# Kernel optimization log

Measured on AMD Instinct MI355X. Metric: run time of the kernel, lower is better.

Reference implementation:

```python
import jax, jax.numpy as jnp
import numpy as np

N_TOKENS = 16384
DIM = 2048
N_EXPERTS = 64
TOPK = 8
ROUTE_SCALE = 1.0


def setup_inputs() -> dict:
    key = jax.random.key(0)
    k1, k2 = jax.random.split(key)
    x = jax.random.normal(k1, (N_TOKENS, DIM), dtype=jnp.float32)
    W = jax.random.normal(k2, (N_EXPERTS, DIM), dtype=jnp.float32) * 0.02
    return {"x": x, "W": W}


def reference(x, W):
    # linear scores: [tokens, n_experts]
    logits = jnp.einsum('td,ed->te', x, W)
    # softmax in float32 (score_func == 'softmax'); bias is None since dim != 64
    scores = jax.nn.softmax(logits.astype(jnp.float32), axis=-1)
    # top-k expert selection, then gather original scores at selected indices
    _, indices = jax.lax.top_k(scores, TOPK)
    weights = jnp.take_along_axis(scores, indices, axis=-1)
    # softmax path: no renormalization, just route scaling
    weights = (weights * ROUTE_SCALE).astype(x.dtype)
    return weights, indices
```

## Files before the change

kernel.cpp:

```cpp
#include <hip/hip_runtime.h>


typedef __attribute__((ext_vector_type(8))) short short8;
typedef __attribute__((ext_vector_type(16))) float f32x16;
typedef __attribute__((ext_vector_type(4))) float f32x4;
typedef __attribute__((ext_vector_type(4))) unsigned int u32x4;

#define NT    16384
#define DIMK  2048
#define NE    64
#define TOPKK 8
#define WPK_BYTES 786432
#define PL_BYTES  (4 * NT * NE * 4)
#define WS_NEED   (WPK_BYTES + PL_BYTES)

union U4S8 { unsigned int u[4]; short8 s; u32x4 v; };

__device__ __forceinline__ short8 as_s8(u32x4 v) { U4S8 t; t.v = v; return t.s; }

__device__ __forceinline__ void split3(const float4 a, const float4 b,
                                       short8& H, short8& M, short8& L) {
    const float f[8] = {a.x, a.y, a.z, a.w, b.x, b.y, b.z, b.w};
    U4S8 uh, um, ul;
#pragma unroll
    for (int p = 0; p < 4; ++p) {
        const float f0 = f[2 * p], f1 = f[2 * p + 1];
        const unsigned int t0 = __float_as_uint(f0) & 0xFFFF0000u;
        const unsigned int t1 = __float_as_uint(f1) & 0xFFFF0000u;
        uh.u[p] = (t0 >> 16) | t1;
        const float r0 = f0 - __uint_as_float(t0);
        const float r1 = f1 - __uint_as_float(t1);
        const unsigned int v0 = __float_as_uint(r0) & 0xFFFF0000u;
        const unsigned int v1 = __float_as_uint(r1) & 0xFFFF0000u;
        um.u[p] = (v0 >> 16) | v1;
        const float s0 = r0 - __uint_as_float(v0);
        const float s1 = r1 - __uint_as_float(v1);
        ul.u[p] = (__float_as_uint(s0) >> 16) | (__float_as_uint(s1) & 0xFFFF0000u);
    }
    H = uh.s; M = um.s; L = ul.s;
}

__device__ __forceinline__ f32x16 mfma6w(short8 ah, short8 am, short8 al,
                                         short8 bh, short8 bm, short8 bl,
                                         f32x16 c) {
    c = __builtin_amdgcn_mfma_f32_32x32x16_bf16(ah, bh, c, 0, 0, 0);
    c = __builtin_amdgcn_mfma_f32_32x32x16_bf16(ah, bm, c, 0, 0, 0);
    c = __builtin_amdgcn_mfma_f32_32x32x16_bf16(am, bh, c, 0, 0, 0);
    c = __builtin_amdgcn_mfma_f32_32x32x16_bf16(ah, bl, c, 0, 0, 0);
    c = __builtin_amdgcn_mfma_f32_32x32x16_bf16(am, bm, c, 0, 0, 0);
    c = __builtin_amdgcn_mfma_f32_32x32x16_bf16(al, bh, c, 0, 0, 0);
    return c;
}

__global__ __launch_bounds__(64) void pack_w_kernel(
    const float* __restrict__ W, short* __restrict__ wpk)
{
    const int b  = blockIdx.x;
    const int c  = b >> 3, fg = b & 7;
    const int s  = fg >> 1, n32 = fg & 1;
    const int l  = threadIdx.x;
    const float* g = W + (size_t)(32 * n32 + (l & 31)) * DIMK
                       + 64 * c + 16 * s + 8 * (l >> 5);
    const float4 lo = *(const float4*)g;
    const float4 hi = *(const float4*)(g + 4);
    short8 H, M, L;
    split3(lo, hi, H, M, L);
    const size_t base = ((size_t)(c * 8 + fg) * 3) * 512 + l * 8;
    *(short8*)(wpk + base)        = H;
    *(short8*)(wpk + base + 512)  = M;
    *(short8*)(wpk + base + 1024) = L;
}

#define WLOAD3(d0, d1, d2, p)                                                 \
    asm volatile("global_load_dwordx4 %0, %3, off\n\t"                        \
                 "global_load_dwordx4 %1, %3, off offset:1024\n\t"            \
                 "global_load_dwordx4 %2, %3, off offset:2048"                \
                 : "=&v"(d0), "=&v"(d1), "=&v"(d2) : "v"(p))
#define WAITN(n) do {                                                         \
    asm volatile("s_waitcnt vmcnt(" #n ")" ::: "memory");                     \
    __builtin_amdgcn_sched_barrier(0);                                        \
} while (0)

__device__ __forceinline__ void async16(void* lds, const void* gp) {
    __builtin_amdgcn_global_load_lds(
        (const __attribute__((address_space(1))) unsigned int*)gp,
        (__attribute__((address_space(3))) unsigned int*)lds, 16, 0, 0);
}

__global__ __launch_bounds__(512, 1) void gate_ksplit_kernel(
    const float* __restrict__ x, const short* __restrict__ wpk,
    float* __restrict__ pl)
{
    __shared__ __align__(16) char smem[8 * 3 * 4096];

    const int tid = threadIdx.x;
    const int w   = tid >> 6;
    const int l   = tid & 63;
    const int r31 = l & 31;
    const int l5  = l >> 5;
    const int tg  = blockIdx.x >> 2;
    const int kq  = blockIdx.x & 3;
    const int bt0 = tg * 256;
    const int tokbase = bt0 + 32 * w;

    char* wbase = smem + w * 12288;
    const int swr = (r31 & 7) ^ (((r31 >> 3) & 3) << 1);
    const int srow = l >> 3;
    const int sg0  = (l & 7) ^ srow;
    const float* xrow0 = x + (size_t)(tokbase + srow) * DIMK + kq * 512;

#define STAGE_CHUNK(k) do {                                                   \
    _Pragma("unroll")                                                         \
    for (int i = 0; i < 4; ++i) {                                             \
        const float* gsrc = xrow0 + (size_t)(8 * i) * DIMK + (k) * 32         \
                          + ((sg0 ^ (2 * i)) << 2);                           \
        async16(wbase + ((k) % 3) * 4096 + i * 1024, gsrc);                   \
    }                                                                         \
} while (0)

    const short* wq0 = wpk + (size_t)kq * 98304 + l * 8;
    const short* wq1 = wq0 + 1536;

    f32x16 acc0, acc1;
#pragma unroll
    for (int i = 0; i < 16; ++i) { acc0[i] = 0.f; acc1[i] = 0.f; }

    u32x4 w0v[4][3], w1v[4][3];

    STAGE_CHUNK(0);
    STAGE_CHUNK(1);
    STAGE_CHUNK(2);
    WLOAD3(w0v[0][0], w0v[0][1], w0v[0][2], wq0); wq0 += 3072;
    WLOAD3(w1v[0][0], w1v[0][1], w1v[0][2], wq1); wq1 += 3072;
    WLOAD3(w0v[1][0], w0v[1][1], w0v[1][2], wq0); wq0 += 3072;
    WLOAD3(w1v[1][0], w1v[1][1], w1v[1][2], wq1); wq1 += 3072;
    WLOAD3(w0v[2][0], w0v[2][1], w0v[2][2], wq0); wq0 += 3072;
    WLOAD3(w1v[2][0], w1v[2][1], w1v[2][2], wq1); wq1 += 3072;

#define SLICE(t) do {                                                         \
    if ((t) <= 28) {                                                          \
        WLOAD3(w0v[((t)+3)&3][0], w0v[((t)+3)&3][1], w0v[((t)+3)&3][2], wq0); \
        wq0 += 3072;                                                          \
        WLOAD3(w1v[((t)+3)&3][0], w1v[((t)+3)&3][1], w1v[((t)+3)&3][2], wq1); \
        wq1 += 3072;                                                          \
    }                                                                         \
    if ((t) <= 1)            WAITN(18);                                       \
    else if ((t) == 29)      WAITN(12);                                       \
    else if ((t) == 30)      WAITN(6);                                        \
    else if ((t) == 31)      WAITN(0);                                        \
    else if (((t) & 1) || (t) == 2 || (t) == 28) WAITN(22);                   \
    else                     WAITN(26);                                       \
    {                                                                         \
        const char* xb = wbase + (((t) >> 1) % 3) * 4096;                     \
        const float4 a0 = *(const float4*)(xb + r31 * 128 +                   \
            (((((t) & 1) * 4 + 2 * l5 + 0) ^ swr) << 4));                     \
        const float4 a1 = *(const float4*)(xb + r31 * 128 +                   \
            (((((t) & 1) * 4 + 2 * l5 + 1) ^ swr) << 4));                     \
        short8 H, M, L;                                                       \
        split3(a0, a1, H, M, L);                                              \
        acc0 = mfma6w(H, M, L, as_s8(w0v[(t)&3][0]), as_s8(w0v[(t)&3][1]),    \
                      as_s8(w0v[(t)&3][2]), acc0);                            \
        acc1 = mfma6w(H, M, L, as_s8(w1v[(t)&3][0]), as_s8(w1v[(t)&3][1]),    \
                      as_s8(w1v[(t)&3][2]), acc1);                            \
    }                                                                         \
    if (((t) & 1) && (t) <= 25) STAGE_CHUNK(((t) + 5) >> 1);                  \
} while (0)

#define PBAR() __builtin_amdgcn_s_barrier()

    SLICE(0);  SLICE(1);  PBAR();
    SLICE(2);  SLICE(3);  PBAR();
    SLICE(4);  SLICE(5);  PBAR();
    SLICE(6);  SLICE(7);  PBAR();
    SLICE(8);  SLICE(9);  PBAR();
    SLICE(10); SLICE(11); PBAR();
    SLICE(12); SLICE(13); PBAR();
    SLICE(14); SLICE(15); PBAR();
    SLICE(16); SLICE(17); PBAR();
    SLICE(18); SLICE(19); PBAR();
    SLICE(20); SLICE(21); PBAR();
    SLICE(22); SLICE(23); PBAR();
    SLICE(24); SLICE(25); PBAR();
    SLICE(26); SLICE(27); PBAR();
    SLICE(28); SLICE(29); PBAR();
    SLICE(30); SLICE(31);

    float* base0 = pl + ((size_t)kq * NT + tokbase) * NE;
#pragma unroll
    for (int r = 0; r < 16; ++r) {
        const int rowc = (r & 3) + 8 * (r >> 2) + 4 * l5;
        base0[rowc * NE + r31]      = acc0[r];
        base0[rowc * NE + 32 + r31] = acc1[r];
    }
#undef SLICE
#undef STAGE_CHUNK
#undef PBAR
}

__global__ __launch_bounds__(128) void gate_combine_kernel(
    const float* __restrict__ pl, float* __restrict__ out)
{
    __shared__ float lgs[128][NE + 1];

    const int tid = threadIdx.x;
    const int t0  = blockIdx.x * 128;

#pragma unroll
    for (int i = 0; i < 16; ++i) {
        const int idx = i * 128 + tid;
        const int tok = idx >> 4, c4 = idx & 15;
        const size_t off = ((size_t)t0 + tok) * NE + c4 * 4;
        const f32x4 v0 = *(const f32x4*)(pl + off);
        const f32x4 v1 = *(const f32x4*)(pl + (size_t)NT * NE + off);
        const f32x4 v2 = *(const f32x4*)(pl + (size_t)2 * NT * NE + off);
        const f32x4 v3 = *(const f32x4*)(pl + (size_t)3 * NT * NE + off);
        const f32x4 s = (v0 + v1) + (v2 + v3);
#pragma unroll
        for (int j = 0; j < 4; ++j) lgs[tok][c4 * 4 + j] = s[j];
    }
    __syncthreads();

    const float* rowp = &lgs[tid][0];
    float mx = -3.402823466e38f;
    for (int e = 0; e < NE; ++e) mx = fmaxf(mx, rowp[e]);
    float sden = 0.f;
    for (int e = 0; e < NE; ++e) sden += expf(rowp[e] - mx);

    float tv[TOPKK];
    int   ti[TOPKK];
#pragma unroll
    for (int i = 0; i < TOPKK; ++i) { tv[i] = -3.402823466e38f; ti[i] = 0; }
    for (int e = 0; e < NE; ++e) {
        const float v = rowp[e];
        if (v > tv[TOPKK - 1]) {
            tv[TOPKK - 1] = v; ti[TOPKK - 1] = e;
#pragma unroll
            for (int q = TOPKK - 1; q > 0; --q) {
                if (tv[q] > tv[q - 1]) {
                    const float fv = tv[q]; tv[q] = tv[q - 1]; tv[q - 1] = fv;
                    const int   iv = ti[q]; ti[q] = ti[q - 1]; ti[q - 1] = iv;
                }
            }
        }
    }

    float* ow = out + (size_t)(t0 + tid) * TOPKK;
    float* oi = out + (size_t)NT * TOPKK + (size_t)(t0 + tid) * TOPKK;
#pragma unroll
    for (int i = 0; i < TOPKK; ++i) {
        ow[i] = expf(tv[i] - mx) / sden;
        oi[i] = (float)ti[i];
    }
}

__global__ __launch_bounds__(512, 1) void gate_main_r8(
    const float* __restrict__ x, const short* __restrict__ wpk,
    float* __restrict__ out)
{
    __shared__ __align__(16) char smem[8 * 3 * 4096];
    const int tid = threadIdx.x;
    const int w   = tid >> 6;
    const int l   = tid & 63;
    const int r31 = l & 31;
    const int l5  = l >> 5;
    const int tw  = w & 1;
    const int kq  = w >> 1;
    const int bt0 = blockIdx.x * 64;
    char* wbase = smem + w * 12288;
    const int swr = (r31 & 7) ^ (((r31 >> 3) & 3) << 1);
    const int srow = l >> 3;
    const int sg0  = (l & 7) ^ srow;
    const float* xrow0 = x + (size_t)(bt0 + 32 * tw + srow) * DIMK + kq * 512;

#define STAGE_CHUNK(k) do {                                                   \
    _Pragma("unroll")                                                         \
    for (int i = 0; i < 4; ++i) {                                             \
        const float* gsrc = xrow0 + (size_t)(8 * i) * DIMK + (k) * 32         \
                          + ((sg0 ^ (2 * i)) << 2);                           \
        async16(wbase + ((k) % 3) * 4096 + i * 1024, gsrc);                   \
    }                                                                         \
} while (0)

    const short* wq0 = wpk + (size_t)kq * 98304 + l * 8;
    const short* wq1 = wq0 + 1536;
    f32x16 acc0, acc1;
#pragma unroll
    for (int i = 0; i < 16; ++i) { acc0[i] = 0.f; acc1[i] = 0.f; }
    u32x4 w0v[4][3], w1v[4][3];
    STAGE_CHUNK(0); STAGE_CHUNK(1); STAGE_CHUNK(2);
    WLOAD3(w0v[0][0], w0v[0][1], w0v[0][2], wq0); wq0 += 3072;
    WLOAD3(w1v[0][0], w1v[0][1], w1v[0][2], wq1); wq1 += 3072;
    WLOAD3(w0v[1][0], w0v[1][1], w0v[1][2], wq0); wq0 += 3072;
    WLOAD3(w1v[1][0], w1v[1][1], w1v[1][2], wq1); wq1 += 3072;
    WLOAD3(w0v[2][0], w0v[2][1], w0v[2][2], wq0); wq0 += 3072;
    WLOAD3(w1v[2][0], w1v[2][1], w1v[2][2], wq1); wq1 += 3072;

#define SLICE(t) do {                                                         \
    if ((t) <= 28) {                                                          \
        WLOAD3(w0v[((t)+3)&3][0], w0v[((t)+3)&3][1], w0v[((t)+3)&3][2], wq0); \
        wq0 += 3072;                                                          \
        WLOAD3(w1v[((t)+3)&3][0], w1v[((t)+3)&3][1], w1v[((t)+3)&3][2], wq1); \
        wq1 += 3072;                                                          \
    }                                                                         \
    if ((t) <= 1)            WAITN(18);                                       \
    else if ((t) == 29)      WAITN(12);                                       \
    else if ((t) == 30)      WAITN(6);                                        \
    else if ((t) == 31)      WAITN(0);                                        \
    else if (((t) & 1) || (t) == 2 || (t) == 28) WAITN(22);                   \
    else                     WAITN(26);                                       \
    {                                                                         \
        const char* xb = wbase + (((t) >> 1) % 3) * 4096;                     \
        const float4 a0 = *(const float4*)(xb + r31 * 128 +                   \
            (((((t) & 1) * 4 + 2 * l5 + 0) ^ swr) << 4));                     \
        const float4 a1 = *(const float4*)(xb + r31 * 128 +                   \
            (((((t) & 1) * 4 + 2 * l5 + 1) ^ swr) << 4));                     \
        short8 H, M, L;                                                       \
        split3(a0, a1, H, M, L);                                              \
        acc0 = mfma6w(H, M, L, as_s8(w0v[(t)&3][0]), as_s8(w0v[(t)&3][1]),    \
                      as_s8(w0v[(t)&3][2]), acc0);                            \
        acc1 = mfma6w(H, M, L, as_s8(w1v[(t)&3][0]), as_s8(w1v[(t)&3][1]),    \
                      as_s8(w1v[(t)&3][2]), acc1);                            \
    }                                                                         \
    if (((t) & 1) && (t) <= 25) STAGE_CHUNK(((t) + 5) >> 1);                  \
} while (0)

    SLICE(0);  SLICE(1);  SLICE(2);  SLICE(3);
    SLICE(4);  SLICE(5);  SLICE(6);  SLICE(7);
    SLICE(8);  SLICE(9);  SLICE(10); SLICE(11);
    SLICE(12); SLICE(13); SLICE(14); SLICE(15);
    SLICE(16); SLICE(17); SLICE(18); SLICE(19);
    SLICE(20); SLICE(21); SLICE(22); SLICE(23);
    SLICE(24); SLICE(25); SLICE(26); SLICE(27);
    SLICE(28); SLICE(29); SLICE(30); SLICE(31);

    __syncthreads();
    float* lg = (float*)smem;
#pragma unroll
    for (int r = 0; r < 16; ++r) {
        const int rowc = (r & 3) + 8 * (r >> 2) + 4 * l5;
        const int trow = 32 * tw + rowc;
        lg[(kq * 64 + trow) * (NE + 1) + r31]      = acc0[r];
        lg[(kq * 64 + trow) * (NE + 1) + 32 + r31] = acc1[r];
    }
    __syncthreads();
#pragma unroll
    for (int rr = 0; rr < 8; ++rr) {
        const int idx = tid + rr * 512;
        const int t = idx >> 6, e = idx & 63;
        lg[t * (NE + 1) + e] =
            (lg[t * (NE + 1) + e] + lg[(64 + t) * (NE + 1) + e]) +
            (lg[(128 + t) * (NE + 1) + e] + lg[(192 + t) * (NE + 1) + e]);
    }
    __syncthreads();
    if (tid < 64) {
        const float* rowp = lg + tid * (NE + 1);
        float mx = -3.402823466e38f;
        for (int e = 0; e < NE; ++e) mx = fmaxf(mx, rowp[e]);
        float sden = 0.f;
        for (int e = 0; e < NE; ++e) sden += expf(rowp[e] - mx);
        float tv[TOPKK]; int ti[TOPKK];
#pragma unroll
        for (int i = 0; i < TOPKK; ++i) { tv[i] = -3.402823466e38f; ti[i] = 0; }
        for (int e = 0; e < NE; ++e) {
            const float v = rowp[e];
            if (v > tv[TOPKK - 1]) {
                tv[TOPKK - 1] = v; ti[TOPKK - 1] = e;
#pragma unroll
                for (int q = TOPKK - 1; q > 0; --q) {
                    if (tv[q] > tv[q - 1]) {
                        const float fv = tv[q]; tv[q] = tv[q - 1]; tv[q - 1] = fv;
                        const int   iv = ti[q]; ti[q] = ti[q - 1]; ti[q - 1] = iv;
                    }
                }
            }
        }
        float* ow = out + (size_t)(bt0 + tid) * TOPKK;
        float* oi = out + (size_t)NT * TOPKK + (size_t)(bt0 + tid) * TOPKK;
#pragma unroll
        for (int i = 0; i < TOPKK; ++i) {
            ow[i] = expf(tv[i] - mx) / sden;
            oi[i] = (float)ti[i];
        }
    }
#undef SLICE
#undef STAGE_CHUNK
}

extern "C" void kernel_launch(void* const* d_in, const int* in_sizes, int n_in,
                              void* d_out, int out_size, void* d_ws, size_t ws_size,
                              hipStream_t stream) {
    const float* x = (const float*)d_in[0];
    const float* W = (const float*)d_in[1];
    float* out = (float*)d_out;
    short* wpk = (short*)d_ws;
    if (ws_size >= (size_t)WS_NEED) {
        float* pl = (float*)((char*)d_ws + WPK_BYTES);
        hipLaunchKernelGGL(pack_w_kernel, dim3(256), dim3(64), 0, stream, W, wpk);
        hipLaunchKernelGGL(gate_ksplit_kernel, dim3(256), dim3(512), 0, stream,
                           x, wpk, pl);
        hipLaunchKernelGGL(gate_combine_kernel, dim3(NT / 128), dim3(128), 0, stream,
                           pl, out);
    } else if (ws_size >= (size_t)WPK_BYTES) {
        hipLaunchKernelGGL(pack_w_kernel, dim3(256), dim3(64), 0, stream, W, wpk);
        hipLaunchKernelGGL(gate_main_r8, dim3(NT / 64), dim3(512), 0, stream,
                           x, wpk, out);
    }
}
```

Measured before the change: 59.03 us.

## Share packed W tiles across waves via LDS in k-split gate kernel

In the k-split gate kernel, each wave used to load its own copy of the packed bf16-split W slices from global memory into registers. Now six waves cooperatively stage each W chunk into a 4-deep LDS ring with async global-to-LDS loads, and all eight waves read it from shared memory. This cuts redundant global/L2 traffic for W and frees the registers that held the prefetched W. The cost is a block-wide barrier every chunk, extra LDS reads, and 144 KB of dynamic LDS per block.

New measurement: 57.11 us. 1.03x faster.

```diff
diff --git a/kernel.cpp b/kernel.cpp
--- a/kernel.cpp
+++ b/kernel.cpp
@@ -13,6 +13,7 @@
 #define WPK_BYTES 786432
 #define PL_BYTES  (4 * NT * NE * 4)
 #define WS_NEED   (WPK_BYTES + PL_BYTES)
+#define KS2_LDS   (4 * 12288 + 8 * 12288)
 
 union U4S8 { unsigned int u[4]; short8 s; u32x4 v; };
 
@@ -71,13 +72,13 @@
     *(short8*)(wpk + base + 1024) = L;
 }
 
-#define WLOAD3(d0, d1, d2, p)                                                 \
-    asm volatile("global_load_dwordx4 %0, %3, off\n\t"                        \
-                 "global_load_dwordx4 %1, %3, off offset:1024\n\t"            \
-                 "global_load_dwordx4 %2, %3, off offset:2048"                \
-                 : "=&v"(d0), "=&v"(d1), "=&v"(d2) : "v"(p))
 #define WAITN(n) do {                                                         \
     asm volatile("s_waitcnt vmcnt(" #n ")" ::: "memory");                     \
+    __builtin_amdgcn_sched_barrier(0);                                        \
+} while (0)
+#define BAR() do {                                                            \
+    __builtin_amdgcn_sched_barrier(0);                                        \
+    __builtin_amdgcn_s_barrier();                                             \
     __builtin_amdgcn_sched_barrier(0);                                        \
 } while (0)
 
@@ -87,11 +88,11 @@
         (__attribute__((address_space(3))) unsigned int*)lds, 16, 0, 0);
 }
 
-__global__ __launch_bounds__(512, 1) void gate_ksplit_kernel(
+__global__ __launch_bounds__(512, 1) void gate_ksplit2_kernel(
     const float* __restrict__ x, const short* __restrict__ wpk,
     float* __restrict__ pl)
 {
-    __shared__ __align__(16) char smem[8 * 3 * 4096];
+    extern __shared__ __align__(16) char smem[];
 
     const int tid = threadIdx.x;
     const int w   = tid >> 6;
@@ -100,14 +101,182 @@
     const int l5  = l >> 5;
     const int tg  = blockIdx.x >> 2;
     const int kq  = blockIdx.x & 3;
-    const int bt0 = tg * 256;
-    const int tokbase = bt0 + 32 * w;
-
-    char* wbase = smem + w * 12288;
+    const int tokbase = tg * 256 + 32 * w;
+
+    char* xbase = smem + 49152 + w * 12288;
     const int swr = (r31 & 7) ^ (((r31 >> 3) & 3) << 1);
     const int srow = l >> 3;
     const int sg0  = (l & 7) ^ srow;
     const float* xrow0 = x + (size_t)(tokbase + srow) * DIMK + kq * 512;
+
+#define KS2_STAGE_X(k) do {                                                   \
+    _Pragma("unroll")                                                         \
+    for (int i = 0; i < 4; ++i) {                                             \
+        const float* gsrc = xrow0 + (size_t)(8 * i) * DIMK + (k) * 32         \
+                          + ((sg0 ^ (2 * i)) << 2);                           \
+        async16(xbase + ((k) % 3) * 4096 + i * 1024, gsrc);                   \
+    }                                                                         \
+} while (0)
+
+#define KS2_STAGE_W(cc) do {                                                  \
+    if (w < 6) {                                                              \
+        _Pragma("unroll")                                                     \
+        for (int rr = 0; rr < 2; ++rr) {                                      \
+            const int r   = 2 * w + rr;                                       \
+            const int ss  = (r >= 6) ? 1 : 0;                                 \
+            const int rm  = r - 6 * ss;                                       \
+            const int n32 = (rm >= 3) ? 1 : 0;                                \
+            const int t   = rm - 3 * n32;                                     \
+            const int fg  = 2 * (2 * ((cc) & 1) + ss) + n32;                  \
+            const int c64g = kq * 8 + ((cc) >> 1);                            \
+            const short* gs = wpk + ((size_t)(c64g * 8 + fg) * 3 + t) * 512   \
+                            + l * 8;                                          \
+            async16(smem + ((cc) & 3) * 12288 + r * 1024, gs);                \
+        }                                                                     \
+    }                                                                         \
+} while (0)
+
+#define KS2_COMPUTE(cc) do {                                                  \
+    const char* xb = xbase + ((cc) % 3) * 4096;                               \
+    const char* wb = smem + ((cc) & 3) * 12288;                               \
+    _Pragma("unroll")                                                         \
+    for (int ss = 0; ss < 2; ++ss) {                                          \
+        const float4 a0 = *(const float4*)(xb + r31 * 128 +                   \
+            (((4 * ss + 2 * l5 + 0) ^ swr) << 4));                            \
+        const float4 a1 = *(const float4*)(xb + r31 * 128 +                   \
+            (((4 * ss + 2 * l5 + 1) ^ swr) << 4));                            \
+        short8 H, M, L;                                                       \
+        split3(a0, a1, H, M, L);                                              \
+        const char* wsl = wb + ss * 6144 + l * 16;                            \
+        const short8 b00 = *(const short8*)(wsl);                             \
+        const short8 b01 = *(const short8*)(wsl + 1024);                      \
+        const short8 b02 = *(const short8*)(wsl + 2048);                      \
+        const short8 b10 = *(const short8*)(wsl + 3072);                      \
+        const short8 b11 = *(const short8*)(wsl + 4096);                      \
+        const short8 b12 = *(const short8*)(wsl + 5120);                      \
+        acc0 = mfma6w(H, M, L, b00, b01, b02, acc0);                          \
+        acc1 = mfma6w(H, M, L, b10, b11, b12, acc1);                          \
+    }                                                                         \
+} while (0)
+
+#define KS2_ITER(c) do {                                                      \
+    if ((c) <= 13) KS2_STAGE_W((c) + 2);                                      \
+    if ((c) <= 13)      { if (w < 6) WAITN(12); else WAITN(8); }              \
+    else if ((c) == 14) { if (w < 6) WAITN(6);  else WAITN(4); }              \
+    else                { WAITN(0); }                                         \
+    BAR();                                                                    \
+    KS2_COMPUTE(c);                                                           \
+    if ((c) <= 12) KS2_STAGE_X((c) + 3);                                      \
+} while (0)
+
+    f32x16 acc0, acc1;
+#pragma unroll
+    for (int i = 0; i < 16; ++i) { acc0[i] = 0.f; acc1[i] = 0.f; }
+
+    KS2_STAGE_X(0);
+    KS2_STAGE_W(0);
+    KS2_STAGE_X(1);
+    KS2_STAGE_W(1);
+    KS2_STAGE_X(2);
+
+    KS2_ITER(0);  KS2_ITER(1);  KS2_ITER(2);  KS2_ITER(3);
+    KS2_ITER(4);  KS2_ITER(5);  KS2_ITER(6);  KS2_ITER(7);
+    KS2_ITER(8);  KS2_ITER(9);  KS2_ITER(10); KS2_ITER(11);
+    KS2_ITER(12); KS2_ITER(13); KS2_ITER(14); KS2_ITER(15);
+
+    float* base0 = pl + ((size_t)kq * NT + tokbase) * NE;
+#pragma unroll
+    for (int r = 0; r < 16; ++r) {
+        const int rowc = (r & 3) + 8 * (r >> 2) + 4 * l5;
+        base0[rowc * NE + r31]      = acc0[r];
+        base0[rowc * NE + 32 + r31] = acc1[r];
+    }
+#undef KS2_ITER
+#undef KS2_COMPUTE
+#undef KS2_STAGE_W
+#undef KS2_STAGE_X
+}
+
+__global__ __launch_bounds__(128) void gate_combine_kernel(
+    const float* __restrict__ pl, float* __restrict__ out)
+{
+    __shared__ float lgs[128][NE + 1];
+
+    const int tid = threadIdx.x;
+    const int t0  = blockIdx.x * 128;
+
+#pragma unroll
+    for (int i = 0; i < 16; ++i) {
+        const int idx = i * 128 + tid;
+        const int tok = idx >> 4, c4 = idx & 15;
+        const size_t off = ((size_t)t0 + tok) * NE + c4 * 4;
+        const f32x4 v0 = *(const f32x4*)(pl + off);
+        const f32x4 v1 = *(const f32x4*)(pl + (size_t)NT * NE + off);
+        const f32x4 v2 = *(const f32x4*)(pl + (size_t)2 * NT * NE + off);
+        const f32x4 v3 = *(const f32x4*)(pl + (size_t)3 * NT * NE + off);
+        const f32x4 s = (v0 + v1) + (v2 + v3);
+#pragma unroll
+        for (int j = 0; j < 4; ++j) lgs[tok][c4 * 4 + j] = s[j];
+    }
+    __syncthreads();
+
+    const float* rowp = &lgs[tid][0];
+    float mx = -3.402823466e38f;
+    for (int e = 0; e < NE; ++e) mx = fmaxf(mx, rowp[e]);
+    float sden = 0.f;
+    for (int e = 0; e < NE; ++e) sden += expf(rowp[e] - mx);
+
+    float tv[TOPKK];
+    int   ti[TOPKK];
+#pragma unroll
+    for (int i = 0; i < TOPKK; ++i) { tv[i] = -3.402823466e38f; ti[i] = 0; }
+    for (int e = 0; e < NE; ++e) {
+        const float v = rowp[e];
+        if (v > tv[TOPKK - 1]) {
+            tv[TOPKK - 1] = v; ti[TOPKK - 1] = e;
+#pragma unroll
+            for (int q = TOPKK - 1; q > 0; --q) {
+                if (tv[q] > tv[q - 1]) {
+                    const float fv = tv[q]; tv[q] = tv[q - 1]; tv[q - 1] = fv;
+                    const int   iv = ti[q]; ti[q] = ti[q - 1]; ti[q - 1] = iv;
+                }
+            }
+        }
+    }
+
+    float* ow = out + (size_t)(t0 + tid) * TOPKK;
+    float* oi = out + (size_t)NT * TOPKK + (size_t)(t0 + tid) * TOPKK;
+#pragma unroll
+    for (int i = 0; i < TOPKK; ++i) {
+        ow[i] = expf(tv[i] - mx) / sden;
+        oi[i] = (float)ti[i];
+    }
+}
+
+#define WLOAD3(d0, d1, d2, p)                                                 \
+    asm volatile("global_load_dwordx4 %0, %3, off\n\t"                        \
+                 "global_load_dwordx4 %1, %3, off offset:1024\n\t"            \
+                 "global_load_dwordx4 %2, %3, off offset:2048"                \
+                 : "=&v"(d0), "=&v"(d1), "=&v"(d2) : "v"(p))
+
+__global__ __launch_bounds__(512, 1) void gate_main_r8(
+    const float* __restrict__ x, const short* __restrict__ wpk,
+    float* __restrict__ out)
+{
+    __shared__ __align__(16) char smem8[8 * 3 * 4096];
+    const int tid = threadIdx.x;
+    const int w   = tid >> 6;
+    const int l   = tid & 63;
+    const int r31 = l & 31;
+    const int l5  = l >> 5;
+    const int tw  = w & 1;
+    const int kq  = w >> 1;
+    const int bt0 = blockIdx.x * 64;
+    char* wbase = smem8 + w * 12288;
+    const int swr = (r31 & 7) ^ (((r31 >> 3) & 3) << 1);
+    const int srow = l >> 3;
+    const int sg0  = (l & 7) ^ srow;
+    const float* xrow0 = x + (size_t)(bt0 + 32 * tw + srow) * DIMK + kq * 512;
 
 #define STAGE_CHUNK(k) do {                                                   \
     _Pragma("unroll")                                                         \
@@ -120,16 +289,11 @@
 
     const short* wq0 = wpk + (size_t)kq * 98304 + l * 8;
     const short* wq1 = wq0 + 1536;
-
     f32x16 acc0, acc1;
 #pragma unroll
     for (int i = 0; i < 16; ++i) { acc0[i] = 0.f; acc1[i] = 0.f; }
-
     u32x4 w0v[4][3], w1v[4][3];
-
-    STAGE_CHUNK(0);
-    STAGE_CHUNK(1);
-    STAGE_CHUNK(2);
+    STAGE_CHUNK(0); STAGE_CHUNK(1); STAGE_CHUNK(2);
     WLOAD3(w0v[0][0], w0v[0][1], w0v[0][2], wq0); wq0 += 3072;
     WLOAD3(w1v[0][0], w1v[0][1], w1v[0][2], wq1); wq1 += 3072;
     WLOAD3(w0v[1][0], w0v[1][1], w0v[1][2], wq0); wq0 += 3072;
@@ -166,164 +330,6 @@
     if (((t) & 1) && (t) <= 25) STAGE_CHUNK(((t) + 5) >> 1);                  \
 } while (0)
 
-#define PBAR() __builtin_amdgcn_s_barrier()
-
-    SLICE(0);  SLICE(1);  PBAR();
-    SLICE(2);  SLICE(3);  PBAR();
-    SLICE(4);  SLICE(5);  PBAR();
-    SLICE(6);  SLICE(7);  PBAR();
-    SLICE(8);  SLICE(9);  PBAR();
-    SLICE(10); SLICE(11); PBAR();
-    SLICE(12); SLICE(13); PBAR();
-    SLICE(14); SLICE(15); PBAR();
-    SLICE(16); SLICE(17); PBAR();
-    SLICE(18); SLICE(19); PBAR();
-    SLICE(20); SLICE(21); PBAR();
-    SLICE(22); SLICE(23); PBAR();
-    SLICE(24); SLICE(25); PBAR();
-    SLICE(26); SLICE(27); PBAR();
-    SLICE(28); SLICE(29); PBAR();
-    SLICE(30); SLICE(31);
-
-    float* base0 = pl + ((size_t)kq * NT + tokbase) * NE;
-#pragma unroll
-    for (int r = 0; r < 16; ++r) {
-        const int rowc = (r & 3) + 8 * (r >> 2) + 4 * l5;
-        base0[rowc * NE + r31]      = acc0[r];
-        base0[rowc * NE + 32 + r31] = acc1[r];
-    }
-#undef SLICE
-#undef STAGE_CHUNK
-#undef PBAR
-}
-
-__global__ __launch_bounds__(128) void gate_combine_kernel(
-    const float* __restrict__ pl, float* __restrict__ out)
-{
-    __shared__ float lgs[128][NE + 1];
-
-    const int tid = threadIdx.x;
-    const int t0  = blockIdx.x * 128;
-
-#pragma unroll
-    for (int i = 0; i < 16; ++i) {
-        const int idx = i * 128 + tid;
-        const int tok = idx >> 4, c4 = idx & 15;
-        const size_t off = ((size_t)t0 + tok) * NE + c4 * 4;
-        const f32x4 v0 = *(const f32x4*)(pl + off);
-        const f32x4 v1 = *(const f32x4*)(pl + (size_t)NT * NE + off);
-        const f32x4 v2 = *(const f32x4*)(pl + (size_t)2 * NT * NE + off);
-        const f32x4 v3 = *(const f32x4*)(pl + (size_t)3 * NT * NE + off);
-        const f32x4 s = (v0 + v1) + (v2 + v3);
-#pragma unroll
-        for (int j = 0; j < 4; ++j) lgs[tok][c4 * 4 + j] = s[j];
-    }
-    __syncthreads();
-
-    const float* rowp = &lgs[tid][0];
-    float mx = -3.402823466e38f;
-    for (int e = 0; e < NE; ++e) mx = fmaxf(mx, rowp[e]);
-    float sden = 0.f;
-    for (int e = 0; e < NE; ++e) sden += expf(rowp[e] - mx);
-
-    float tv[TOPKK];
-    int   ti[TOPKK];
-#pragma unroll
-    for (int i = 0; i < TOPKK; ++i) { tv[i] = -3.402823466e38f; ti[i] = 0; }
-    for (int e = 0; e < NE; ++e) {
-        const float v = rowp[e];
-        if (v > tv[TOPKK - 1]) {
-            tv[TOPKK - 1] = v; ti[TOPKK - 1] = e;
-#pragma unroll
-            for (int q = TOPKK - 1; q > 0; --q) {
-                if (tv[q] > tv[q - 1]) {
-                    const float fv = tv[q]; tv[q] = tv[q - 1]; tv[q - 1] = fv;
-                    const int   iv = ti[q]; ti[q] = ti[q - 1]; ti[q - 1] = iv;
-                }
-            }
-        }
-    }
-
-    float* ow = out + (size_t)(t0 + tid) * TOPKK;
-    float* oi = out + (size_t)NT * TOPKK + (size_t)(t0 + tid) * TOPKK;
-#pragma unroll
-    for (int i = 0; i < TOPKK; ++i) {
-        ow[i] = expf(tv[i] - mx) / sden;
-        oi[i] = (float)ti[i];
-    }
-}
-
-__global__ __launch_bounds__(512, 1) void gate_main_r8(
-    const float* __restrict__ x, const short* __restrict__ wpk,
-    float* __restrict__ out)
-{
-    __shared__ __align__(16) char smem[8 * 3 * 4096];
-    const int tid = threadIdx.x;
-    const int w   = tid >> 6;
-    const int l   = tid & 63;
-    const int r31 = l & 31;
-    const int l5  = l >> 5;
-    const int tw  = w & 1;
-    const int kq  = w >> 1;
-    const int bt0 = blockIdx.x * 64;
-    char* wbase = smem + w * 12288;
-    const int swr = (r31 & 7) ^ (((r31 >> 3) & 3) << 1);
-    const int srow = l >> 3;
-    const int sg0  = (l & 7) ^ srow;
-    const float* xrow0 = x + (size_t)(bt0 + 32 * tw + srow) * DIMK + kq * 512;
-
-#define STAGE_CHUNK(k) do {                                                   \
-    _Pragma("unroll")                                                         \
-    for (int i = 0; i < 4; ++i) {                                             \
-        const float* gsrc = xrow0 + (size_t)(8 * i) * DIMK + (k) * 32         \
-                          + ((sg0 ^ (2 * i)) << 2);                           \
-        async16(wbase + ((k) % 3) * 4096 + i * 1024, gsrc);                   \
-    }                                                                         \
-} while (0)
-
-    const short* wq0 = wpk + (size_t)kq * 98304 + l * 8;
-    const short* wq1 = wq0 + 1536;
-    f32x16 acc0, acc1;
-#pragma unroll
-    for (int i = 0; i < 16; ++i) { acc0[i] = 0.f; acc1[i] = 0.f; }
-    u32x4 w0v[4][3], w1v[4][3];
-    STAGE_CHUNK(0); STAGE_CHUNK(1); STAGE_CHUNK(2);
-    WLOAD3(w0v[0][0], w0v[0][1], w0v[0][2], wq0); wq0 += 3072;
-    WLOAD3(w1v[0][0], w1v[0][1], w1v[0][2], wq1); wq1 += 3072;
-    WLOAD3(w0v[1][0], w0v[1][1], w0v[1][2], wq0); wq0 += 3072;
-    WLOAD3(w1v[1][0], w1v[1][1], w1v[1][2], wq1); wq1 += 3072;
-    WLOAD3(w0v[2][0], w0v[2][1], w0v[2][2], wq0); wq0 += 3072;
-    WLOAD3(w1v[2][0], w1v[2][1], w1v[2][2], wq1); wq1 += 3072;
-
-#define SLICE(t) do {                                                         \
-    if ((t) <= 28) {                                                          \
-        WLOAD3(w0v[((t)+3)&3][0], w0v[((t)+3)&3][1], w0v[((t)+3)&3][2], wq0); \
-        wq0 += 3072;                                                          \
-        WLOAD3(w1v[((t)+3)&3][0], w1v[((t)+3)&3][1], w1v[((t)+3)&3][2], wq1); \
-        wq1 += 3072;                                                          \
-    }                                                                         \
-    if ((t) <= 1)            WAITN(18);                                       \
-    else if ((t) == 29)      WAITN(12);                                       \
-    else if ((t) == 30)      WAITN(6);                                        \
-    else if ((t) == 31)      WAITN(0);                                        \
-    else if (((t) & 1) || (t) == 2 || (t) == 28) WAITN(22);                   \
-    else                     WAITN(26);                                       \
-    {                                                                         \
-        const char* xb = wbase + (((t) >> 1) % 3) * 4096;                     \
-        const float4 a0 = *(const float4*)(xb + r31 * 128 +                   \
-            (((((t) & 1) * 4 + 2 * l5 + 0) ^ swr) << 4));                     \
-        const float4 a1 = *(const float4*)(xb + r31 * 128 +                   \
-            (((((t) & 1) * 4 + 2 * l5 + 1) ^ swr) << 4));                     \
-        short8 H, M, L;                                                       \
-        split3(a0, a1, H, M, L);                                              \
-        acc0 = mfma6w(H, M, L, as_s8(w0v[(t)&3][0]), as_s8(w0v[(t)&3][1]),    \
-                      as_s8(w0v[(t)&3][2]), acc0);                            \
-        acc1 = mfma6w(H, M, L, as_s8(w1v[(t)&3][0]), as_s8(w1v[(t)&3][1]),    \
-                      as_s8(w1v[(t)&3][2]), acc1);                            \
-    }                                                                         \
-    if (((t) & 1) && (t) <= 25) STAGE_CHUNK(((t) + 5) >> 1);                  \
-} while (0)
-
     SLICE(0);  SLICE(1);  SLICE(2);  SLICE(3);
     SLICE(4);  SLICE(5);  SLICE(6);  SLICE(7);
     SLICE(8);  SLICE(9);  SLICE(10); SLICE(11);
@@ -334,7 +340,7 @@
     SLICE(28); SLICE(29); SLICE(30); SLICE(31);
 
     __syncthreads();
-    float* lg = (float*)smem;
+    float* lg = (float*)smem8;
 #pragma unroll
     for (int r = 0; r < 16; ++r) {
         const int rowc = (r & 3) + 8 * (r >> 2) + 4 * l5;
@@ -396,8 +402,8 @@
     if (ws_size >= (size_t)WS_NEED) {
         float* pl = (float*)((char*)d_ws + WPK_BYTES);
         hipLaunchKernelGGL(pack_w_kernel, dim3(256), dim3(64), 0, stream, W, wpk);
-        hipLaunchKernelGGL(gate_ksplit_kernel, dim3(256), dim3(512), 0, stream,
-                           x, wpk, pl);
+        hipLaunchKernelGGL(gate_ksplit2_kernel, dim3(256), dim3(512),
+                           KS2_LDS, stream, x, wpk, pl);
         hipLaunchKernelGGL(gate_combine_kernel, dim3(NT / 128), dim3(128), 0, stream,
                            pl, out);
     } else if (ws_size >= (size_t)WPK_BYTES) {
```

## Reduce K-split partials in-block, halve partial-logit buffer and combine traffic

Applied to the files above, without the earlier changes.

The main GEMM kernel now assigns two K-quarters per block (two warps per token tile), sums their partial logits in LDS, and writes only two partial buffers instead of four. The combine kernel reads two partials instead of four, which cuts global write and read traffic for the intermediate logits. The barrier cadence is also relaxed from every two slices to every four, and the fallback fused kernel is retuned to 256 threads with 2 blocks per CU. The trade-off is an extra LDS reduction and __syncthreads inside the GEMM kernel, plus a change in how blocks cover tokens.

Measured after the change: 57.07 us. 1.03x faster.

```diff
diff --git a/kernel.cpp b/kernel.cpp
--- a/kernel.cpp
+++ b/kernel.cpp
@@ -11,7 +11,7 @@
 #define NE    64
 #define TOPKK 8
 #define WPK_BYTES 786432
-#define PL_BYTES  (4 * NT * NE * 4)
+#define PL_BYTES  (2 * NT * NE * 4)
 #define WS_NEED   (WPK_BYTES + PL_BYTES)
 
 union U4S8 { unsigned int u[4]; short8 s; u32x4 v; };
@@ -87,7 +87,7 @@
         (__attribute__((address_space(3))) unsigned int*)lds, 16, 0, 0);
 }
 
-__global__ __launch_bounds__(512, 1) void gate_ksplit_kernel(
+__global__ __launch_bounds__(512, 1) void gate_half_kernel(
     const float* __restrict__ x, const short* __restrict__ wpk,
     float* __restrict__ pl)
 {
@@ -98,16 +98,18 @@
     const int l   = tid & 63;
     const int r31 = l & 31;
     const int l5  = l >> 5;
-    const int tg  = blockIdx.x >> 2;
-    const int kq  = blockIdx.x & 3;
-    const int bt0 = tg * 256;
-    const int tokbase = bt0 + 32 * w;
+    const int tw  = w >> 1;
+    const int kq2 = w & 1;
+    const int tgb = blockIdx.x >> 1;
+    const int kh  = blockIdx.x & 1;
+    const int tok0 = tgb * 128 + tw * 32;
+    const int q    = kh * 2 + kq2;
 
     char* wbase = smem + w * 12288;
     const int swr = (r31 & 7) ^ (((r31 >> 3) & 3) << 1);
     const int srow = l >> 3;
     const int sg0  = (l & 7) ^ srow;
-    const float* xrow0 = x + (size_t)(tokbase + srow) * DIMK + kq * 512;
+    const float* xrow0 = x + (size_t)(tok0 + srow) * DIMK + q * 512;
 
 #define STAGE_CHUNK(k) do {                                                   \
     _Pragma("unroll")                                                         \
@@ -118,18 +120,14 @@
     }                                                                         \
 } while (0)
 
-    const short* wq0 = wpk + (size_t)kq * 98304 + l * 8;
+    const short* wq0 = wpk + (size_t)q * 98304 + l * 8;
     const short* wq1 = wq0 + 1536;
-
     f32x16 acc0, acc1;
 #pragma unroll
     for (int i = 0; i < 16; ++i) { acc0[i] = 0.f; acc1[i] = 0.f; }
-
     u32x4 w0v[4][3], w1v[4][3];
 
-    STAGE_CHUNK(0);
-    STAGE_CHUNK(1);
-    STAGE_CHUNK(2);
+    STAGE_CHUNK(0); STAGE_CHUNK(1); STAGE_CHUNK(2);
     WLOAD3(w0v[0][0], w0v[0][1], w0v[0][2], wq0); wq0 += 3072;
     WLOAD3(w1v[0][0], w1v[0][1], w1v[0][2], wq1); wq1 += 3072;
     WLOAD3(w0v[1][0], w0v[1][1], w0v[1][2], wq0); wq0 += 3072;
@@ -168,36 +166,42 @@
 
 #define PBAR() __builtin_amdgcn_s_barrier()
 
-    SLICE(0);  SLICE(1);  PBAR();
-    SLICE(2);  SLICE(3);  PBAR();
-    SLICE(4);  SLICE(5);  PBAR();
-    SLICE(6);  SLICE(7);  PBAR();
-    SLICE(8);  SLICE(9);  PBAR();
-    SLICE(10); SLICE(11); PBAR();
-    SLICE(12); SLICE(13); PBAR();
-    SLICE(14); SLICE(15); PBAR();
-    SLICE(16); SLICE(17); PBAR();
-    SLICE(18); SLICE(19); PBAR();
-    SLICE(20); SLICE(21); PBAR();
-    SLICE(22); SLICE(23); PBAR();
-    SLICE(24); SLICE(25); PBAR();
-    SLICE(26); SLICE(27); PBAR();
-    SLICE(28); SLICE(29); PBAR();
-    SLICE(30); SLICE(31);
-
-    float* base0 = pl + ((size_t)kq * NT + tokbase) * NE;
+    SLICE(0);  SLICE(1);  SLICE(2);  SLICE(3);  PBAR();
+    SLICE(4);  SLICE(5);  SLICE(6);  SLICE(7);  PBAR();
+    SLICE(8);  SLICE(9);  SLICE(10); SLICE(11); PBAR();
+    SLICE(12); SLICE(13); SLICE(14); SLICE(15); PBAR();
+    SLICE(16); SLICE(17); SLICE(18); SLICE(19); PBAR();
+    SLICE(20); SLICE(21); SLICE(22); SLICE(23); PBAR();
+    SLICE(24); SLICE(25); SLICE(26); SLICE(27); PBAR();
+    SLICE(28); SLICE(29); SLICE(30); SLICE(31);
+
+    __syncthreads();
+
+    float* lg = (float*)smem;
 #pragma unroll
     for (int r = 0; r < 16; ++r) {
         const int rowc = (r & 3) + 8 * (r >> 2) + 4 * l5;
-        base0[rowc * NE + r31]      = acc0[r];
-        base0[rowc * NE + 32 + r31] = acc1[r];
+        lg[(w * 32 + rowc) * (NE + 1) + r31]      = acc0[r];
+        lg[(w * 32 + rowc) * (NE + 1) + 32 + r31] = acc1[r];
+    }
+    __syncthreads();
+
+#pragma unroll
+    for (int rr = 0; rr < 16; ++rr) {
+        const int idx = tid + rr * 512;
+        const int t5  = idx >> 6;
+        const int e   = idx & 63;
+        const int tw2 = t5 >> 5, rloc = t5 & 31;
+        const float s = lg[((2 * tw2) * 32 + rloc) * (NE + 1) + e]
+                      + lg[((2 * tw2 + 1) * 32 + rloc) * (NE + 1) + e];
+        pl[((size_t)kh * NT + tgb * 128 + t5) * NE + e] = s;
     }
 #undef SLICE
 #undef STAGE_CHUNK
 #undef PBAR
 }
 
-__global__ __launch_bounds__(128) void gate_combine_kernel(
+__global__ __launch_bounds__(128) void gate_combine2_kernel(
     const float* __restrict__ pl, float* __restrict__ out)
 {
     __shared__ float lgs[128][NE + 1];
@@ -212,9 +216,7 @@
         const size_t off = ((size_t)t0 + tok) * NE + c4 * 4;
         const f32x4 v0 = *(const f32x4*)(pl + off);
         const f32x4 v1 = *(const f32x4*)(pl + (size_t)NT * NE + off);
-        const f32x4 v2 = *(const f32x4*)(pl + (size_t)2 * NT * NE + off);
-        const f32x4 v3 = *(const f32x4*)(pl + (size_t)3 * NT * NE + off);
-        const f32x4 s = (v0 + v1) + (v2 + v3);
+        const f32x4 s = v0 + v1;
 #pragma unroll
         for (int j = 0; j < 4; ++j) lgs[tok][c4 * 4 + j] = s[j];
     }
@@ -253,24 +255,23 @@
     }
 }
 
-__global__ __launch_bounds__(512, 1) void gate_main_r8(
+__global__ __launch_bounds__(256, 2) void gate_main_r12(
     const float* __restrict__ x, const short* __restrict__ wpk,
     float* __restrict__ out)
 {
-    __shared__ __align__(16) char smem[8 * 3 * 4096];
+    __shared__ __align__(16) char smem[4 * 3 * 4096];
     const int tid = threadIdx.x;
     const int w   = tid >> 6;
     const int l   = tid & 63;
     const int r31 = l & 31;
     const int l5  = l >> 5;
-    const int tw  = w & 1;
-    const int kq  = w >> 1;
-    const int bt0 = blockIdx.x * 64;
+    const int kq  = w;
+    const int bt0 = blockIdx.x * 32;
     char* wbase = smem + w * 12288;
     const int swr = (r31 & 7) ^ (((r31 >> 3) & 3) << 1);
     const int srow = l >> 3;
     const int sg0  = (l & 7) ^ srow;
-    const float* xrow0 = x + (size_t)(bt0 + 32 * tw + srow) * DIMK + kq * 512;
+    const float* xrow0 = x + (size_t)(bt0 + srow) * DIMK + kq * 512;
 
 #define STAGE_CHUNK(k) do {                                                   \
     _Pragma("unroll")                                                         \
@@ -338,21 +339,20 @@
 #pragma unroll
     for (int r = 0; r < 16; ++r) {
         const int rowc = (r & 3) + 8 * (r >> 2) + 4 * l5;
-        const int trow = 32 * tw + rowc;
-        lg[(kq * 64 + trow) * (NE + 1) + r31]      = acc0[r];
-        lg[(kq * 64 + trow) * (NE + 1) + 32 + r31] = acc1[r];
+        lg[(w * 32 + rowc) * (NE + 1) + r31]      = acc0[r];
+        lg[(w * 32 + rowc) * (NE + 1) + 32 + r31] = acc1[r];
     }
     __syncthreads();
 #pragma unroll
     for (int rr = 0; rr < 8; ++rr) {
-        const int idx = tid + rr * 512;
+        const int idx = tid + rr * 256;
         const int t = idx >> 6, e = idx & 63;
         lg[t * (NE + 1) + e] =
-            (lg[t * (NE + 1) + e] + lg[(64 + t) * (NE + 1) + e]) +
-            (lg[(128 + t) * (NE + 1) + e] + lg[(192 + t) * (NE + 1) + e]);
-    }
-    __syncthreads();
-    if (tid < 64) {
+            (lg[t * (NE + 1) + e] + lg[(32 + t) * (NE + 1) + e]) +
+            (lg[(64 + t) * (NE + 1) + e] + lg[(96 + t) * (NE + 1) + e]);
+    }
+    __syncthreads();
+    if (tid < 32) {
         const float* rowp = lg + tid * (NE + 1);
         float mx = -3.402823466e38f;
         for (int e = 0; e < NE; ++e) mx = fmaxf(mx, rowp[e]);
@@ -396,13 +396,13 @@
     if (ws_size >= (size_t)WS_NEED) {
         float* pl = (float*)((char*)d_ws + WPK_BYTES);
         hipLaunchKernelGGL(pack_w_kernel, dim3(256), dim3(64), 0, stream, W, wpk);
-        hipLaunchKernelGGL(gate_ksplit_kernel, dim3(256), dim3(512), 0, stream,
+        hipLaunchKernelGGL(gate_half_kernel, dim3(256), dim3(512), 0, stream,
                            x, wpk, pl);
-        hipLaunchKernelGGL(gate_combine_kernel, dim3(NT / 128), dim3(128), 0, stream,
-                           pl, out);
+        hipLaunchKernelGGL(gate_combine2_kernel, dim3(NT / 128), dim3(128), 0,
+                           stream, pl, out);
     } else if (ws_size >= (size_t)WPK_BYTES) {
         hipLaunchKernelGGL(pack_w_kernel, dim3(256), dim3(64), 0, stream, W, wpk);
-        hipLaunchKernelGGL(gate_main_r8, dim3(NT / 64), dim3(512), 0, stream,
+        hipLaunchKernelGGL(gate_main_r12, dim3(NT / 32), dim3(256), 0, stream,
                            x, wpk, out);
     }
 }
```
